# Performance work log

Measured on AMD Instinct MI355X. Metric: run time of the kernel, lower is better.

The kernel has to match this reference:

```python
import jax, jax.numpy as jnp
import numpy as np

B, N = 32, 2048
SLOTS, PSD, VIEW = 5, 15, 9
DM, NH, MH, EGO = 64, 4, 128, 32
PAIR_D = SLOTS * (SLOTS - 1) // 2          # 10
TER_D = VIEW * VIEW                        # 81
NBR_D = SLOTS * PSD + PAIR_D               # 85
D_OBS = EGO + NBR_D + TER_D                # 198


def setup_inputs() -> dict:
    key = jax.random.key(0)
    ks = jax.random.split(key, 64)

    def _p(k, shape, s=0.05):
        return (jax.random.normal(k, shape) * s).astype(jnp.float32)

    def z(*shape):
        return jnp.zeros(shape, jnp.float32)

    # --- observation with some genuinely-masked slots (r == 0) ---
    ego = jax.random.normal(ks[0], (B, N, EGO), jnp.float32)
    nbr = jax.random.normal(ks[1], (B, N, SLOTS, PSD), jnp.float32)
    keep = jax.random.bernoulli(ks[2], 0.8, (B, N, SLOTS)).astype(jnp.float32)
    nbr = jnp.concatenate([nbr[..., 0:3] * keep[..., None], nbr[..., 3:]], axis=-1)
    pair = jax.random.normal(ks[3], (B, N, PAIR_D), jnp.float32)
    ter = jax.random.normal(ks[4], (B, N, TER_D), jnp.float32)
    obs = jnp.concatenate([ego, nbr.reshape(B, N, SLOTS * PSD), pair, ter], axis=-1)

    i = 5
    def nk():
        nonlocal i
        i += 1
        return ks[i - 1]

    params = {
        "tok_w": _p(nk(), (12, DM)), "tok_b": z(DM),
        "ln1_s": jnp.ones((DM,), jnp.float32), "ln1_b": z(DM),
        "a1_qw": _p(nk(), (DM, DM)), "a1_qb": z(DM),
        "a1_kw": _p(nk(), (DM, DM)), "a1_kb": z(DM),
        "a1_vw": _p(nk(), (DM, DM)), "a1_vb": z(DM),
        "a1_ow": _p(nk(), (DM, DM)), "a1_ob": z(DM),
        "ln2_s": jnp.ones((DM,), jnp.float32), "ln2_b": z(DM),
        "m1_w": _p(nk(), (DM, MH)), "m1_b": z(MH),
        "m2_w": _p(nk(), (MH, MH)), "m2_b": z(MH),
        "m3_w": _p(nk(), (MH, DM)), "m3_b": z(DM),
        "e1_w": _p(nk(), (EGO, MH)), "e1_b": z(MH),
        "e2_w": _p(nk(), (MH, MH)), "e2_b": z(MH),
        "e3_w": _p(nk(), (MH, DM)), "e3_b": z(DM),
        "l1_w": _p(nk(), (2 * DM, MH)), "l1_b": z(MH),
        "l2_w": _p(nk(), (MH, MH)), "l2_b": z(MH),
        "l3_w": _p(nk(), (MH, 1)), "l3_b": z(1),
        "seed": _p(nk(), (1, 1, DM), 0.02),
        "p_qw": _p(nk(), (DM, DM)), "p_qb": z(DM),
        "p_kw": _p(nk(), (DM, DM)), "p_kb": z(DM),
        "p_vw": _p(nk(), (DM, DM)), "p_vb": z(DM),
        "p_ow": _p(nk(), (DM, DM)), "p_ob": z(DM),
        "pr_w": _p(nk(), (PAIR_D, DM)), "pr_b": z(DM),
        "h1_w": _p(nk(), (EGO + 2 * DM, MH)), "h1_b": z(MH),
        "h2_w": _p(nk(), (MH, MH)), "h2_b": z(MH),
        "h3_w": _p(nk(), (MH, MH)), "h3_b": z(MH),
    }
    return {"obs": obs, **params}


def _layernorm(x, s, b, eps=1e-6):
    m = jnp.mean(x, axis=-1, keepdims=True)
    v = jnp.var(x, axis=-1, keepdims=True)
    return (x - m) * jax.lax.rsqrt(v + eps) * s + b


def _zero_if_masked(x, mask):
    return jnp.where(mask[..., None], x, jnp.array(0.0, x.dtype))


def _masked_softmax(logits, mask, eps=1e-9):
    mask = mask.astype(bool)
    very_neg = jnp.array(-1e9, logits.dtype)
    ml = jnp.where(mask, logits, very_neg)
    mx = jnp.max(ml, axis=-1, keepdims=True)
    ex = jnp.exp(ml - mx) * mask.astype(logits.dtype)
    return ex / (jnp.sum(ex, axis=-1, keepdims=True) + eps)


def _mha(q_in, kv_in, attn_mask, qw, qb, kw, kb, vw, vb, ow, ob, nh=NH):
    dm = q_in.shape[-1]
    dh = dm // nh
    q = (q_in @ qw + qb).reshape(*q_in.shape[:-1], nh, dh)
    k = (kv_in @ kw + kb).reshape(*kv_in.shape[:-1], nh, dh)
    v = (kv_in @ vw + vb).reshape(*kv_in.shape[:-1], nh, dh)
    logits = jnp.einsum('...qhd,...khd->...hqk', q, k) / jnp.sqrt(jnp.float32(dh))
    neg = jnp.finfo(logits.dtype).min
    logits = jnp.where(attn_mask, logits, neg)
    attn = jax.nn.softmax(logits, axis=-1)
    o = jnp.einsum('...hqk,...khd->...qhd', attn, v).reshape(*q_in.shape[:-1], dm)
    return o @ ow + ob


def _mlp3(x, w1, b1, w2, b2, w3, b3):
    x = jax.nn.gelu(x @ w1 + b1)
    x = jax.nn.gelu(x @ w2 + b2)
    return x @ w3 + b3


def reference(obs, tok_w, tok_b, ln1_s, ln1_b,
              a1_qw, a1_qb, a1_kw, a1_kb, a1_vw, a1_vb, a1_ow, a1_ob,
              ln2_s, ln2_b, m1_w, m1_b, m2_w, m2_b, m3_w, m3_b,
              e1_w, e1_b, e2_w, e2_b, e3_w, e3_b,
              l1_w, l1_b, l2_w, l2_b, l3_w, l3_b,
              seed, p_qw, p_qb, p_kw, p_kb, p_vw, p_vb, p_ow, p_ob,
              pr_w, pr_b, h1_w, h1_b, h2_w, h2_b, h3_w, h3_b):
    obs = obs.astype(jnp.float32)
    Bb, Nn, Dd = obs.shape
    ego = obs[..., :EGO]
    nbr_all = obs[..., EGO:EGO + NBR_D]
    nbr_main = nbr_all[..., :SLOTS * PSD].reshape(Bb, Nn, SLOTS, PSD)
    pair = nbr_all[..., SLOTS * PSD:]

    r = nbr_main[..., 0:3]
    u = nbr_main[..., 3:6]
    att = nbr_main[..., 6:9]
    fre = nbr_main[..., 9:10]
    tem = nbr_main[..., 10:11]
    inv = nbr_main[..., 11:15]

    mask = jnp.any(jnp.abs(r) > 1e-6, axis=-1)                 # (B,N,K)
    mask_any = jnp.any(mask, axis=-1, keepdims=True)           # (B,N,1)
    mask_safe = jnp.where(mask_any, mask, mask.at[..., 0].set(True))

    r_clean = jnp.nan_to_num(r, nan=0.0, posinf=0.0, neginf=0.0)
    diff = r_clean[..., :, None, :] - r_clean[..., None, :, :]
    dist = jnp.linalg.norm(diff, axis=-1)                      # (B,N,K,K)
    pair_mask = mask[..., :, None] & mask[..., None, :]
    eye = jnp.eye(SLOTS, dtype=bool)[None, None]
    valid = pair_mask & ~eye
    big = jnp.array(1e9, dist.dtype)
    dist_no_self = jnp.where(eye, big, dist)
    d_min = jnp.min(jnp.where(valid, dist_no_self, big), axis=-1, keepdims=True)
    d_sum = jnp.sum(jnp.where(valid, dist, 0.0), axis=-1, keepdims=True)
    cnt = jnp.sum(valid, axis=-1, keepdims=True).astype(dist.dtype)
    d_mean = jnp.where(cnt > 0, d_sum / (cnt + 1e-9), 0.0)
    att_norm = jnp.linalg.norm(att, axis=-1, keepdims=True)

    tok_in = jnp.concatenate([inv, fre, tem, att, att_norm, d_min, d_mean], axis=-1)  # (B,N,K,12)
    tok = jax.nn.gelu(tok_in @ tok_w + tok_b)
    tok = _zero_if_masked(tok, mask)

    # --- SetTransformerBlock ---
    qk = mask_safe[..., :, None] & mask_safe[..., None, :]
    attn_mask = qk[..., None, :, :]                            # (B,N,1,K,K)
    y = _layernorm(tok, ln1_s, ln1_b)
    y = _mha(y, y, attn_mask, a1_qw, a1_qb, a1_kw, a1_kb, a1_vw, a1_vb, a1_ow, a1_ob)
    y = _zero_if_masked(y, mask)
    tok = tok + y
    zz = _layernorm(tok, ln2_s, ln2_b)
    zz = _mlp3(zz, m1_w, m1_b, m2_w, m2_b, m3_w, m3_b)
    zz = _zero_if_masked(zz, mask)
    tok = _zero_if_masked(tok + zz, mask)

    # --- alpha weights ---
    ego_ctx = _mlp3(ego, e1_w, e1_b, e2_w, e2_b, e3_w, e3_b)   # (B,N,DM)
    ego_ctx_b = jnp.broadcast_to(ego_ctx[..., None, :], tok.shape)
    logits = _mlp3(jnp.concatenate([tok, ego_ctx_b], axis=-1),
                   l1_w, l1_b, l2_w, l2_b, l3_w, l3_b)[..., 0]
    alpha = _masked_softmax(logits, mask)
    alpha3 = alpha[..., None]
    v_r = jnp.sum(alpha3 * r, axis=-2)
    v_u = jnp.sum(alpha3 * u, axis=-2)

    # --- AttentionPool ---
    q = jnp.broadcast_to(seed, (*tok.shape[:-2], 1, DM)).astype(jnp.float32)
    pool_mask = mask_safe[..., None, None, :]                  # (B,N,1,1,K)
    c = _mha(q, tok, pool_mask, p_qw, p_qb, p_kw, p_kb, p_vw, p_vb, p_ow, p_ob)[..., 0, :]
    c = jnp.where(mask_any, c, jnp.zeros_like(c))

    pair_emb = jax.nn.gelu(pair @ pr_w + pr_b)
    h_in = jnp.concatenate([ego, c, pair_emb], axis=-1)
    h = _mlp3(h_in, h1_w, h1_b, h2_w, h2_b, h3_w, h3_b)
    return jnp.concatenate([h, v_r, v_u], axis=-1)             # (B,N,134)
```

## Files before the change

kernel.cpp:

```cpp
#include <hip/hip_runtime.h>
#include <math.h>


#define DOBS 198
#define NEG_INF_F (-3.402823466e38f)

typedef __bf16 v8bf __attribute__((ext_vector_type(8)));
typedef __bf16 v4bf __attribute__((ext_vector_type(4)));
typedef float  v4f  __attribute__((ext_vector_type(4)));

struct P {
  const float *obs,*tok_w,*tok_b,*ln1_s,*ln1_b,
    *a1_qw,*a1_qb,*a1_kw,*a1_kb,*a1_vw,*a1_vb,*a1_ow,*a1_ob,
    *ln2_s,*ln2_b,*m1_w,*m1_b,*m2_w,*m2_b,*m3_w,*m3_b,
    *e1_w,*e1_b,*e2_w,*e2_b,*e3_w,*e3_b,
    *l1_w,*l1_b,*l2_w,*l2_b,*l3_w,*l3_b,
    *seed,*p_qw,*p_qb,*p_kw,*p_kb,*p_vw,*p_vb,*p_ow,*p_ob,
    *pr_w,*pr_b,*h1_w,*h1_b,*h2_w,*h2_b,*h3_w,*h3_b;
  float* out;
};
static_assert(sizeof(P) == 51*sizeof(void*), "P layout");

#define W_A1Q 0
#define W_A1K 4096
#define W_A1V 8192
#define W_A1O 12288
#define W_M1  16384
#define W_M2  24576
#define W_M3  40960
#define W_E1  49152
#define W_E2  53248
#define W_E3  69632
#define W_L1  77824
#define W_L2  94208
#define W_PK  110592
#define W_PV  114688
#define W_PO  118784
#define W_H1  122880
#define W_H2  143360
#define W_H3  159744
#define W_END 176128
#define W_QP  176128

__global__ __launch_bounds__(256)
void prep_w(P a, __bf16* ws)
{
  if (blockIdx.x == 172){
    int t = threadIdx.x;
    if (t < 64){
      float acc = a.p_qb[t];
      for (int k=0;k<64;k++) acc += a.seed[k]*a.p_qw[k*64+t];
      ((float*)(ws + W_QP))[t] = acc;
    }
    return;
  }
  const float* srcs[18] = {a.a1_qw,a.a1_kw,a.a1_vw,a.a1_ow,a.m1_w,a.m2_w,a.m3_w,
                           a.e1_w,a.e2_w,a.e3_w,a.l1_w,a.l2_w,a.p_kw,a.p_vw,a.p_ow,
                           a.h1_w,a.h2_w,a.h3_w};
  const int Ks[18]   = {64,64,64,64,64,128,128,32,128,128,128,128,64,64,64,160,128,128};
  const int Ns[18]   = {64,64,64,64,128,128,64,128,128,64,128,128,64,64,64,128,128,128};
  const int offs[18] = {W_A1Q,W_A1K,W_A1V,W_A1O,W_M1,W_M2,W_M3,W_E1,W_E2,W_E3,
                        W_L1,W_L2,W_PK,W_PV,W_PO,W_H1,W_H2,W_H3};
  __shared__ float tile[32][33];
  int b = blockIdx.x, m = 0, acc = 0;
  for (; m < 18; m++){
    int t = (Ks[m]/32)*(Ns[m]/32);
    if (b < acc + t) break;
    acc += t;
  }
  int lt = b - acc, K = Ks[m], N = Ns[m];
  int ntile = N/32, kt = lt/ntile, nt = lt%ntile;
  int tx = threadIdx.x & 31, ty = threadIdx.x >> 5;
  const float* S = srcs[m];
  #pragma unroll
  for (int rr=0; rr<32; rr+=8)
    tile[ty+rr][tx] = S[(size_t)(kt*32+ty+rr)*N + nt*32+tx];
  __syncthreads();
  __bf16* D = ws + offs[m];
  #pragma unroll
  for (int rr=0; rr<32; rr+=8)
    D[(size_t)(nt*32+ty+rr)*K + kt*32+tx] = (__bf16)tile[tx][ty+rr];
}

__device__ __forceinline__ float gelu_f(float x){
  float t = x * fmaf(0.0356774081f, x*x, 0.7978845608f);
  float u = __builtin_amdgcn_exp2f(-2.885390082f * t);
  return x * __builtin_amdgcn_rcpf(1.0f + u);
}

__device__ __forceinline__ void load16f(const __bf16* p, float* f){
  v8bf a = *(const v8bf*)p, b = *(const v8bf*)(p+8);
  #pragma unroll
  for (int i=0;i<8;i++){ f[i]=(float)a[i]; f[8+i]=(float)b[i]; }
}

template<int KT,int MT,int NTPW,typename LA,typename E>
__device__ __forceinline__ void gemmNS(LA la, const __bf16* __restrict__ Wt,
    const float* __restrict__ bias, int wv, int lane, E epi)
{
  const int ar = lane&15, quad = lane>>4;
  #pragma unroll
  for (int ln=0; ln<NTPW; ln++){
    const int wt = wv*NTPW + ln;
    const __bf16* wp = Wt + (size_t)(wt*16+ar)*(KT*32) + quad*8;
    v8bf wf[KT];
    #pragma unroll
    for (int kt=0;kt<KT;kt++) wf[kt] = *(const v8bf*)(wp + kt*32);
    float4 b4 = *(const float4*)(bias + wt*16 + quad*4);
    #pragma unroll
    for (int mt=0; mt<MT; mt++){
      v4f c; c[0]=b4.x; c[1]=b4.y; c[2]=b4.z; c[3]=b4.w;
      #pragma unroll
      for (int kt=0;kt<KT;kt++)
        c = __builtin_amdgcn_mfma_f32_16x16x32_bf16(wf[kt], la(mt,kt,ar,quad), c, 0,0,0);
      epi(wt*16 + quad*4, mt, ar, c);
    }
  }
}

__global__ __launch_bounds__(256,3)
void swarm_mfma(P a, const __bf16* __restrict__ ws, int ntok)
{
  __shared__ char smem[53120] __attribute__((aligned(16)));
  __bf16* Ab   = (__bf16*)(smem);
  __bf16* Bb   = (__bf16*)(smem+17408);
  float*  TOKIN= (float*) (smem+17408);
  __bf16* Tk   = (__bf16*)(smem+34816);
  float*  OBSf = (float*) (smem+34816);
  __bf16* Po   = (__bf16*)(smem+34816);
  __bf16* Pe   = (__bf16*)(smem+44032);
  __bf16* Eg   = (__bf16*)(smem+46080);
  __bf16* Ru   = (__bf16*)(smem+47360);
  __bf16* mfb  = (__bf16*)(smem+48096);
  __bf16* msfb = (__bf16*)(smem+48224);
  float*  many = (float*) (smem+48352);
  float*  lga  = (float*) (smem+48416);
  __bf16* ECX  = (__bf16*)(smem+48672);
  float*  pattn= (float*) (smem+48672);
  __bf16* ATTb = (__bf16*)(smem+50720);
  __bf16* Cc   = (__bf16*)(smem+50720);

  const int lane = threadIdx.x & 63;
  const int wv   = threadIdx.x >> 6;
  const int ar   = lane & 15, quad = lane >> 4;
  const long blkT0 = (long)blockIdx.x*12;

  for (int it=lane; it<3*117; it+=64){
    int tg=it/117, c=it-tg*117;
    long gt = blkT0 + 3*wv + tg; if (gt>ntok-1) gt=ntok-1;
    OBSf[(3*wv+tg)*120+c] = a.obs[gt*DOBS+c];
  }
  float* Df = (float*)Ab;
  for (int it=lane; it<75; it+=64){
    int tg=it/25, p=it-tg*25, i=p/5, j=p-i*5;
    const float* ob = OBSf + (3*wv+tg)*120 + 32;
    float d2=0.f;
    #pragma unroll
    for (int d=0;d<3;d++){
      float ri=ob[15*i+d]; ri = isfinite(ri)?ri:0.f;
      float rj=ob[15*j+d]; rj = isfinite(rj)?rj:0.f;
      float df=ri-rj; d2 += df*df;
    }
    Df[(3*wv+tg)*32+p]=sqrtf(d2);
  }
  if (lane<15){
    int T=3*wv+lane/5, s=lane%5;
    const float* b = OBSf + T*120 + 32 + 15*s;
    mfb[15*wv+lane] = (__bf16)((fabsf(b[0])>1e-6f||fabsf(b[1])>1e-6f||fabsf(b[2])>1e-6f)?1.f:0.f);
  }
  if (wv==0 && lane>=60){ mfb[lane]=(__bf16)0.f; msfb[lane]=(__bf16)0.f; }
  if (wv==0 && lane>=12 && lane<16) many[lane]=0.f;
  if (lane<3){
    int T=3*wv+lane;
    float any = (float)mfb[T*5]+(float)mfb[T*5+1]+(float)mfb[T*5+2]+(float)mfb[T*5+3]+(float)mfb[T*5+4];
    float anyf = (any>0.f)?1.f:0.f; many[T]=anyf;
    #pragma unroll
    for (int i=0;i<5;i++) msfb[T*5+i] = (anyf>0.f)? mfb[T*5+i] : (__bf16)((i==0)?1.f:0.f);
  }
  if (lane<15){
    int T=3*wv+lane/5, i=lane%5, R=15*wv+lane;
    float dmin=1e9f,dsum=0.f,cnt=0.f;
    #pragma unroll
    for (int j=0;j<5;j++){
      if (j!=i && (float)mfb[T*5+i]>0.5f && (float)mfb[T*5+j]>0.5f){
        float dd=Df[T*32+i*5+j];
        dmin=fminf(dmin,dd); dsum+=dd; cnt+=1.f;
      }
    }
    TOKIN[R*12+10]=dmin;
    TOKIN[R*12+11]=(cnt>0.f)? dsum/(cnt+1e-9f) : 0.f;
  }
  for (int it=lane; it<150; it+=64){
    int tg=it/50, q=it-tg*50, s=q/10, c=q-s*10;
    int T=3*wv+tg;
    const float* b = OBSf + T*120 + 32 + 15*s;
    float v;
    if (c<4)        v=b[11+c];
    else if (c==4)  v=b[9];
    else if (c==5)  v=b[10];
    else if (c<9)   v=b[6+(c-6)];
    else { float a0=b[6],a1=b[7],a2=b[8]; v=sqrtf(a0*a0+a1*a1+a2*a2); }
    TOKIN[(T*5+s)*12+c]=v;
  }
  for (int it=lane; it<96; it+=64){
    int tg=it>>5, c=it&31;
    Eg[(3*wv+tg)*40+c] = (__bf16)OBSf[(3*wv+tg)*120+c];
  }
  for (int it=lane; it<90; it+=64){
    int tg=it/30, c=it-tg*30;
    Ru[(3*wv+tg)*30+c] = (__bf16)OBSf[(3*wv+tg)*120+32+15*(c/6)+(c%6)];
  }
  for (int it=lane; it<192; it+=64){
    int tg=it>>6, c=it&63;
    float acc = a.pr_b[c];
    #pragma unroll
    for (int k=0;k<10;k++) acc += OBSf[(3*wv+tg)*120+107+k]*a.pr_w[k*64+c];
    Pe[(3*wv+tg)*64+c] = (__bf16)gelu_f(acc);
  }
  __syncthreads();

  {
    float w0[12];
    #pragma unroll
    for (int k=0;k<12;k++) w0[k] = a.tok_w[k*64+lane];
    float tb = a.tok_b[lane];
    for (int r=0;r<15;r++){
      int R = 15*wv + r;
      const float4* tin = (const float4*)(TOKIN + R*12);
      float4 x0 = tin[0], x1 = tin[1], x2 = tin[2];
      float acc = tb;
      acc=fmaf(x0.x,w0[0],acc); acc=fmaf(x0.y,w0[1],acc);
      acc=fmaf(x0.z,w0[2],acc); acc=fmaf(x0.w,w0[3],acc);
      acc=fmaf(x1.x,w0[4],acc); acc=fmaf(x1.y,w0[5],acc);
      acc=fmaf(x1.z,w0[6],acc); acc=fmaf(x1.w,w0[7],acc);
      acc=fmaf(x2.x,w0[8],acc); acc=fmaf(x2.y,w0[9],acc);
      acc=fmaf(x2.z,w0[10],acc); acc=fmaf(x2.w,w0[11],acc);
      Tk[R*72+lane] = (__bf16)(gelu_f(acc)*(float)mfb[R]);
    }
  }
  if (ar<15){
    int R = 15*wv + ar;
    float x[16]; load16f(Tk + R*72 + quad*16, x);
    float s=0.f;
    #pragma unroll
    for (int i=0;i<16;i++) s += x[i];
    s += __shfl_xor(s,16,64); s += __shfl_xor(s,32,64);
    float m = s*(1.f/64.f), q=0.f;
    #pragma unroll
    for (int i=0;i<16;i++){ float d=x[i]-m; q=fmaf(d,d,q); }
    q += __shfl_xor(q,16,64); q += __shfl_xor(q,32,64);
    float rs = __builtin_amdgcn_rsqf(q*(1.f/64.f)+1e-6f);
    v8bf o0,o1;
    #pragma unroll
    for (int i=0;i<8;i++){
      o0[i]=(__bf16)((x[i]  -m)*rs*a.ln1_s[quad*16+i]  +a.ln1_b[quad*16+i]);
      o1[i]=(__bf16)((x[8+i]-m)*rs*a.ln1_s[quad*16+8+i]+a.ln1_b[quad*16+8+i]);
    }
    *(v8bf*)(Ab+R*136+quad*16)=o0; *(v8bf*)(Ab+R*136+quad*16+8)=o1;
  }
  __syncthreads();

  auto actAb = [&](int mt,int kt,int r,int q){ return *(const v8bf*)(Ab + (size_t)(mt*16+r)*136 + q*8 + kt*32); };
  auto actBb = [&](int mt,int kt,int r,int q){ return *(const v8bf*)(Bb + (size_t)(mt*16+r)*136 + q*8 + kt*32); };
  auto actTk = [&](int mt,int kt,int r,int q){ return *(const v8bf*)(Tk + (size_t)(mt*16+r)*72  + q*8 + kt*32); };

  gemmNS<2,4,1>(actAb, ws+W_A1K, a.a1_kb, wv, lane,
    [&](int wb,int mt,int r,v4f c){ v4bf o;
      #pragma unroll
      for (int k=0;k<4;k++) o[k]=(__bf16)c[k];
      *(v4bf*)&Bb[(mt*16+r)*136+64+wb]=o; });
  gemmNS<2,4,1>(actAb, ws+W_A1V, a.a1_vb, wv, lane,
    [&](int wb,int mt,int r,v4f c){ v4bf o;
      #pragma unroll
      for (int k=0;k<4;k++) o[k]=(__bf16)c[k];
      *(v4bf*)&Ab[(mt*16+r)*136+64+wb]=o; });
  gemmNS<2,4,1>(actAb, ws+W_A1Q, a.a1_qb, wv, lane,
    [&](int wb,int mt,int r,v4f c){ v4bf o;
      #pragma unroll
      for (int k=0;k<4;k++) o[k]=(__bf16)c[k];
      *(v4bf*)&Bb[(mt*16+r)*136+wb]=o; });
  __syncthreads();

  if (lane<60){
    int tg=lane/20, rem=lane-tg*20, h=rem/5, i=rem-h*5;
    int T=3*wv+tg;
    bool mi = (float)msfb[T*5+i]>0.5f;
    float qv[16]; load16f(&Bb[(T*5+i)*136 + h*16], qv);
    float lgv[5], mx=NEG_INF_F;
    #pragma unroll
    for (int j=0;j<5;j++){
      float kk[16]; load16f(&Bb[(T*5+j)*136 + 64 + h*16], kk);
      float d=0.f;
      #pragma unroll
      for (int dd=0;dd<16;dd++) d += qv[dd]*kk[dd];
      bool mj = (float)msfb[T*5+j]>0.5f;
      lgv[j] = (mi&&mj)? d*0.25f : NEG_INF_F;
      mx = fmaxf(mx,lgv[j]);
    }
    float sum=0.f, ex[5];
    #pragma unroll
    for (int j=0;j<5;j++){ ex[j]=__expf(lgv[j]-mx); sum+=ex[j]; }
    float inv=1.0f/sum;
    #pragma unroll
    for (int j=0;j<5;j++) ATTb[T*100+(h*5+i)*5+j]=(__bf16)(ex[j]*inv);
  }
  {
    int h = lane>>4;
    #pragma unroll
    for (int tg=0; tg<3; tg++){
      int T=3*wv+tg;
      float v5[5];
      #pragma unroll
      for (int j=0;j<5;j++) v5[j] = (float)Ab[(T*5+j)*136+64+lane];
      #pragma unroll
      for (int i=0;i<5;i++){
        float o=0.f;
        #pragma unroll
        for (int j=0;j<5;j++) o += (float)ATTb[T*100+(h*5+i)*5+j]*v5[j];
        Ab[(T*5+i)*136+lane]=(__bf16)o;
      }
    }
  }
  __syncthreads();

  gemmNS<2,4,1>(actAb, ws+W_A1O, a.a1_ob, wv, lane,
    [&](int wb,int mt,int r,v4f c){
      int R=mt*16+r; float mm=(float)mfb[R];
      v4bf old=*(const v4bf*)&Tk[R*72+wb]; v4bf o;
      #pragma unroll
      for (int k=0;k<4;k++) o[k]=(__bf16)((float)old[k]+c[k]*mm);
      *(v4bf*)&Tk[R*72+wb]=o; });
  __syncthreads();

  if (ar<15){
    int R = 15*wv + ar;
    float x[16]; load16f(Tk + R*72 + quad*16, x);
    float s=0.f;
    #pragma unroll
    for (int i=0;i<16;i++) s += x[i];
    s += __shfl_xor(s,16,64); s += __shfl_xor(s,32,64);
    float m = s*(1.f/64.f), q=0.f;
    #pragma unroll
    for (int i=0;i<16;i++){ float d=x[i]-m; q=fmaf(d,d,q); }
    q += __shfl_xor(q,16,64); q += __shfl_xor(q,32,64);
    float rs = __builtin_amdgcn_rsqf(q*(1.f/64.f)+1e-6f);
    v8bf o0,o1;
    #pragma unroll
    for (int i=0;i<8;i++){
      o0[i]=(__bf16)((x[i]  -m)*rs*a.ln2_s[quad*16+i]  +a.ln2_b[quad*16+i]);
      o1[i]=(__bf16)((x[8+i]-m)*rs*a.ln2_s[quad*16+8+i]+a.ln2_b[quad*16+8+i]);
    }
    *(v8bf*)(Ab+R*136+quad*16)=o0; *(v8bf*)(Ab+R*136+quad*16+8)=o1;
  }
  __syncthreads();

  gemmNS<2,4,2>(actAb, ws+W_M1, a.m1_b, wv, lane,
    [&](int wb,int mt,int r,v4f c){ v4bf o;
      #pragma unroll
      for (int k=0;k<4;k++) o[k]=(__bf16)gelu_f(c[k]);
      *(v4bf*)&Bb[(mt*16+r)*136+wb]=o; });
  __syncthreads();
  gemmNS<4,4,2>(actBb, ws+W_M2, a.m2_b, wv, lane,
    [&](int wb,int mt,int r,v4f c){ v4bf o;
      #pragma unroll
      for (int k=0;k<4;k++) o[k]=(__bf16)gelu_f(c[k]);
      *(v4bf*)&Ab[(mt*16+r)*136+wb]=o; });
  __syncthreads();
  gemmNS<4,4,1>(actAb, ws+W_M3, a.m3_b, wv, lane,
    [&](int wb,int mt,int r,v4f c){
      int R=mt*16+r; float mm=(float)mfb[R];
      v4bf old=*(const v4bf*)&Tk[R*72+wb]; v4bf o;
      #pragma unroll
      for (int k=0;k<4;k++) o[k]=(__bf16)(((float)old[k]+c[k]*mm)*mm);
      *(v4bf*)&Tk[R*72+wb]=o; });
  gemmNS<1,1,2>([&](int,int,int r,int q){ return *(const v8bf*)(Eg + (size_t)r*40 + q*8); },
    ws+W_E1, a.e1_b, wv, lane,
    [&](int wb,int mt,int r,v4f c){ v4bf o;
      #pragma unroll
      for (int k=0;k<4;k++) o[k]=(__bf16)gelu_f(c[k]);
      *(v4bf*)&Bb[r*136+wb]=o; });
  __syncthreads();
  gemmNS<4,1,2>(actBb, ws+W_E2, a.e2_b, wv, lane,
    [&](int wb,int mt,int r,v4f c){ v4bf o;
      #pragma unroll
      for (int k=0;k<4;k++) o[k]=(__bf16)gelu_f(c[k]);
      *(v4bf*)&Ab[r*136+wb]=o; });
  __syncthreads();
  gemmNS<4,1,1>(actAb, ws+W_E3, a.e3_b, wv, lane,
    [&](int wb,int mt,int r,v4f c){ v4bf o;
      #pragma unroll
      for (int k=0;k<4;k++) o[k]=(__bf16)c[k];
      *(v4bf*)&ECX[r*64+wb]=o; });
  __syncthreads();
  gemmNS<4,4,2>([&](int mt,int kt,int r,int q){
      int R=mt*16+r;
      return (kt<2) ? *(const v8bf*)(Tk + (size_t)R*72 + q*8 + kt*32)
                    : *(const v8bf*)(ECX + (size_t)((R*205)>>10)*64 + q*8 + (kt-2)*32); },
    ws+W_L1, a.l1_b, wv, lane,
    [&](int wb,int mt,int r,v4f c){ v4bf o;
      #pragma unroll
      for (int k=0;k<4;k++) o[k]=(__bf16)gelu_f(c[k]);
      *(v4bf*)&Bb[(mt*16+r)*136+wb]=o; });
  __syncthreads();
  gemmNS<4,4,2>(actBb, ws+W_L2, a.l2_b, wv, lane,
    [&](int wb,int mt,int r,v4f c){ v4bf o;
      #pragma unroll
      for (int k=0;k<4;k++) o[k]=(__bf16)gelu_f(c[k]);
      *(v4bf*)&Ab[(mt*16+r)*136+wb]=o; });
  __syncthreads();

  if (ar<15){
    int R = 15*wv + ar;
    float x[16], y[16];
    load16f(&Ab[R*136 + quad*32], x);
    load16f(&Ab[R*136 + quad*32 + 16], y);
    const float* w = a.l3_w + quad*32;
    float p = 0.f;
    #pragma unroll
    for (int i=0;i<16;i++) p = fmaf(x[i], w[i], p);
    #pragma unroll
    for (int i=0;i<16;i++) p = fmaf(y[i], w[16+i], p);
    p += __shfl_xor(p,16,64); p += __shfl_xor(p,32,64);
    if (quad==0) lga[R] = p + a.l3_b[0];
  }
  gemmNS<2,4,1>(actTk, ws+W_PK, a.p_kb, wv, lane,
    [&](int wb,int mt,int r,v4f c){ v4bf o;
      #pragma unroll
      for (int k=0;k<4;k++) o[k]=(__bf16)c[k];
      *(v4bf*)&Bb[(mt*16+r)*136+wb]=o; });
  gemmNS<2,4,1>(actTk, ws+W_PV, a.p_vb, wv, lane,
    [&](int wb,int mt,int r,v4f c){ v4bf o;
      #pragma unroll
      for (int k=0;k<4;k++) o[k]=(__bf16)c[k];
      *(v4bf*)&Bb[(mt*16+r)*136+64+wb]=o; });
  if (lane<3){
    int T=3*wv+lane;
    float ml[5], mx=-1e9f;
    #pragma unroll
    for (int i=0;i<5;i++){ ml[i]=((float)mfb[T*5+i]>0.5f)? lga[T*5+i] : -1e9f; mx=fmaxf(mx,ml[i]); }
    float den=0.f, e[5];
    #pragma unroll
    for (int i=0;i<5;i++){ e[i]=__expf(ml[i]-mx)*(float)mfb[T*5+i]; den+=e[i]; }
    float inv=1.0f/(den+1e-9f);
    #pragma unroll
    for (int i=0;i<5;i++) lga[T*5+i]=e[i]*inv;
  }
  if (lane<18){
    int tg=lane/6, c=lane-tg*6;
    int T=3*wv+tg;
    float v=0.f;
    #pragma unroll
    for (int i=0;i<5;i++) v += lga[T*5+i]*(float)Ru[T*30+i*6+c];
    long tk = blkT0 + T;
    if (tk<ntok) a.out[tk*134+128+c]=v;
  }
  __syncthreads();

  if (lane<12){
    const float* qg = (const float*)(ws + W_QP);
    int tg=lane>>2, h=lane&3;
    int T=3*wv+tg;
    float qv[16];
    #pragma unroll
    for (int dd=0;dd<16;dd++) qv[dd]=qg[h*16+dd];
    float lgv[5], mx=NEG_INF_F;
    #pragma unroll
    for (int j=0;j<5;j++){
      float kk[16]; load16f(&Bb[(T*5+j)*136 + h*16], kk);
      float d=0.f;
      #pragma unroll
      for (int dd=0;dd<16;dd++) d += qv[dd]*kk[dd];
      lgv[j] = ((float)msfb[T*5+j]>0.5f)? d*0.25f : NEG_INF_F;
      mx = fmaxf(mx,lgv[j]);
    }
    float sum=0.f, ex[5];
    #pragma unroll
    for (int j=0;j<5;j++){ ex[j]=__expf(lgv[j]-mx); sum+=ex[j]; }
    float inv=1.0f/sum;
    #pragma unroll
    for (int j=0;j<5;j++) pattn[T*20+h*5+j]=ex[j]*inv;
  }
  for (int it=lane; it<192; it+=64){
    int tg=it>>6, c=it&63, h=c>>4;
    int T=3*wv+tg;
    float o=0.f;
    #pragma unroll
    for (int j=0;j<5;j++)
      o += pattn[T*20+h*5+j]*(float)Bb[(T*5+j)*136+64+c];
    Po[T*64+c]=(__bf16)o;
  }
  __syncthreads();

  gemmNS<2,1,1>([&](int,int kt,int r,int q){ return *(const v8bf*)(Po + (size_t)r*64 + q*8 + kt*32); },
    ws+W_PO, a.p_ob, wv, lane,
    [&](int wb,int mt,int r,v4f c){
      float mm = many[r];
      v4bf o;
      #pragma unroll
      for (int k=0;k<4;k++) o[k]=(__bf16)(c[k]*mm);
      *(v4bf*)&Cc[r*64+wb]=o; });
  __syncthreads();

  gemmNS<5,1,2>([&](int,int kt,int r,int q){
      if (kt==0) return *(const v8bf*)(Eg + (size_t)r*40 + q*8);
      if (kt<3)  return *(const v8bf*)(Cc + (size_t)r*64 + q*8 + (kt-1)*32);
      return *(const v8bf*)(Pe + (size_t)r*64 + q*8 + (kt-3)*32); },
    ws+W_H1, a.h1_b, wv, lane,
    [&](int wb,int mt,int r,v4f c){ v4bf o;
      #pragma unroll
      for (int k=0;k<4;k++) o[k]=(__bf16)gelu_f(c[k]);
      *(v4bf*)&Bb[r*136+wb]=o; });
  __syncthreads();
  gemmNS<4,1,2>(actBb, ws+W_H2, a.h2_b, wv, lane,
    [&](int wb,int mt,int r,v4f c){ v4bf o;
      #pragma unroll
      for (int k=0;k<4;k++) o[k]=(__bf16)gelu_f(c[k]);
      *(v4bf*)&Ab[r*136+wb]=o; });
  __syncthreads();
  gemmNS<4,1,2>(actAb, ws+W_H3, a.h3_b, wv, lane,
    [&](int wb,int mt,int r,v4f c){
      long tk = blkT0 + r;
      if (r<12 && tk<ntok){
        float2* o2 = (float2*)&a.out[tk*134 + wb];
        o2[0] = make_float2(c[0], c[1]);
        o2[1] = make_float2(c[2], c[3]);
      } });
}

extern "C" void kernel_launch(void* const* d_in, const int* in_sizes, int n_in,
                              void* d_out, int out_size, void* d_ws, size_t ws_size,
                              hipStream_t stream)
{
  P a;
  const float** pp = reinterpret_cast<const float**>(&a);
  for (int i=0;i<50;i++) pp[i] = reinterpret_cast<const float*>(d_in[i]);
  a.out = reinterpret_cast<float*>(d_out);
  int ntok = in_sizes[0] / DOBS;

  __bf16* ws = reinterpret_cast<__bf16*>(d_ws);
  hipLaunchKernelGGL(prep_w, dim3(173), dim3(256), 0, stream, a, ws);
  hipLaunchKernelGGL(swarm_mfma, dim3((ntok+11)/12), dim3(256), 0, stream, a, ws, ntok);
}
```

Measured before the change: 513.3 us.

## Split GEMM work across M and N per wave and fuse QKV/KV projections

The shared MFMA GEMM helper is generalized so each wave takes a 2D (M-group × N-group) tile and can process several weight matrices in one pass. Each activation fragment loaded from LDS is then reused across multiple N tiles and weights. The attention Q/K/V projections and the pooling K/V projections are fused into single calls, and the larger MLP GEMMs now give each wave more N tiles over half the M tiles. This cuts redundant LDS activation reads and adds MFMA independence per load, at the cost of more live registers per wave, which may hurt occupancy under launch_bounds(256,3).

Result: slower. 601.7 us (+17.2%).

```diff
diff --git a/kernel.cpp b/kernel.cpp
--- a/kernel.cpp
+++ b/kernel.cpp
@@ -94,28 +94,63 @@
   for (int i=0;i<8;i++){ f[i]=(float)a[i]; f[8+i]=(float)b[i]; }
 }
 
-template<int KT,int MT,int NTPW,typename LA,typename E>
-__device__ __forceinline__ void gemmNS(LA la, const __bf16* __restrict__ Wt,
-    const float* __restrict__ bias, int wv, int lane, E epi)
+template<int KT,int MT,int NTPW,int MSPL,int NW,typename LA,typename E>
+__device__ __forceinline__ void gemmNS(LA la, const __bf16* const* Ws,
+    const float* const* bs, int wv, int lane, E epi)
 {
+  static_assert(MT % MSPL == 0, "MT % MSPL");
   const int ar = lane&15, quad = lane>>4;
+  constexpr int NWN = 4/MSPL;
+  constexpr int SH  = (NWN==4)?2:((NWN==2)?1:0);
+  constexpr int MTW = MT/MSPL;
+  const int ng = wv & (NWN-1), mg = wv >> SH;
+  v8bf  wf[NW][NTPW][KT];
+  float4 b4[NW][NTPW];
+  #pragma unroll
+  for (int w=0; w<NW; w++)
   #pragma unroll
   for (int ln=0; ln<NTPW; ln++){
-    const int wt = wv*NTPW + ln;
-    const __bf16* wp = Wt + (size_t)(wt*16+ar)*(KT*32) + quad*8;
-    v8bf wf[KT];
-    #pragma unroll
-    for (int kt=0;kt<KT;kt++) wf[kt] = *(const v8bf*)(wp + kt*32);
-    float4 b4 = *(const float4*)(bias + wt*16 + quad*4);
-    #pragma unroll
-    for (int mt=0; mt<MT; mt++){
-      v4f c; c[0]=b4.x; c[1]=b4.y; c[2]=b4.z; c[3]=b4.w;
-      #pragma unroll
-      for (int kt=0;kt<KT;kt++)
-        c = __builtin_amdgcn_mfma_f32_16x16x32_bf16(wf[kt], la(mt,kt,ar,quad), c, 0,0,0);
-      epi(wt*16 + quad*4, mt, ar, c);
-    }
-  }
+    const int wt = ng*NTPW + ln;
+    const __bf16* wp = Ws[w] + (size_t)(wt*16+ar)*(KT*32) + quad*8;
+    #pragma unroll
+    for (int kt=0;kt<KT;kt++) wf[w][ln][kt] = *(const v8bf*)(wp + kt*32);
+    b4[w][ln] = *(const float4*)(bs[w] + wt*16 + quad*4);
+  }
+  #pragma unroll
+  for (int mi=0; mi<MTW; mi++){
+    const int mt = mg*MTW + mi;
+    v4f c[NW][NTPW];
+    #pragma unroll
+    for (int w=0;w<NW;w++)
+    #pragma unroll
+    for (int ln=0;ln<NTPW;ln++){
+      c[w][ln][0]=b4[w][ln].x; c[w][ln][1]=b4[w][ln].y;
+      c[w][ln][2]=b4[w][ln].z; c[w][ln][3]=b4[w][ln].w;
+    }
+    #pragma unroll
+    for (int kt=0;kt<KT;kt++){
+      v8bf av = la(mt,kt,ar,quad);
+      #pragma unroll
+      for (int w=0;w<NW;w++)
+      #pragma unroll
+      for (int ln=0;ln<NTPW;ln++)
+        c[w][ln] = __builtin_amdgcn_mfma_f32_16x16x32_bf16(wf[w][ln][kt], av, c[w][ln], 0,0,0);
+    }
+    #pragma unroll
+    for (int w=0;w<NW;w++)
+    #pragma unroll
+    for (int ln=0;ln<NTPW;ln++)
+      epi(w, (ng*NTPW+ln)*16 + quad*4, mt, ar, c[w][ln]);
+  }
+}
+
+template<int KT,int MT,int NTPW,int MSPL,typename LA,typename E>
+__device__ __forceinline__ void gemm1(LA la, const __bf16* W, const float* b,
+    int wv, int lane, E epi)
+{
+  const __bf16* Ws[1] = {W}; const float* bs[1] = {b};
+  gemmNS<KT,MT,NTPW,MSPL,1>(la, Ws, bs, wv, lane,
+    [&](int, int wb,int mt,int r,v4f c){ epi(wb,mt,r,c); });
 }
 
 __global__ __launch_bounds__(256,3)
@@ -264,21 +299,18 @@
   auto actBb = [&](int mt,int kt,int r,int q){ return *(const v8bf*)(Bb + (size_t)(mt*16+r)*136 + q*8 + kt*32); };
   auto actTk = [&](int mt,int kt,int r,int q){ return *(const v8bf*)(Tk + (size_t)(mt*16+r)*72  + q*8 + kt*32); };
 
-  gemmNS<2,4,1>(actAb, ws+W_A1K, a.a1_kb, wv, lane,
-    [&](int wb,int mt,int r,v4f c){ v4bf o;
-      #pragma unroll
-      for (int k=0;k<4;k++) o[k]=(__bf16)c[k];
-      *(v4bf*)&Bb[(mt*16+r)*136+64+wb]=o; });
-  gemmNS<2,4,1>(actAb, ws+W_A1V, a.a1_vb, wv, lane,
-    [&](int wb,int mt,int r,v4f c){ v4bf o;
-      #pragma unroll
-      for (int k=0;k<4;k++) o[k]=(__bf16)c[k];
-      *(v4bf*)&Ab[(mt*16+r)*136+64+wb]=o; });
-  gemmNS<2,4,1>(actAb, ws+W_A1Q, a.a1_qb, wv, lane,
-    [&](int wb,int mt,int r,v4f c){ v4bf o;
-      #pragma unroll
-      for (int k=0;k<4;k++) o[k]=(__bf16)c[k];
-      *(v4bf*)&Bb[(mt*16+r)*136+wb]=o; });
+  {
+    const __bf16* Ws[3] = {ws+W_A1K, ws+W_A1V, ws+W_A1Q};
+    const float*  bs[3] = {a.a1_kb, a.a1_vb, a.a1_qb};
+    gemmNS<2,4,2,2,3>(actAb, Ws, bs, wv, lane,
+      [&](int w,int wb,int mt,int r,v4f c){ v4bf o;
+        #pragma unroll
+        for (int k=0;k<4;k++) o[k]=(__bf16)c[k];
+        __bf16* d = (w==0)? &Bb[(mt*16+r)*136+64+wb]
+                 : (w==1)? &Ab[(mt*16+r)*136+64+wb]
+                         : &Bb[(mt*16+r)*136+wb];
+        *(v4bf*)d = o; });
+  }
   __syncthreads();
 
   if (lane<60){
@@ -323,7 +355,7 @@
   }
   __syncthreads();
 
-  gemmNS<2,4,1>(actAb, ws+W_A1O, a.a1_ob, wv, lane,
+  gemm1<2,4,2,2>(actAb, ws+W_A1O, a.a1_ob, wv, lane,
     [&](int wb,int mt,int r,v4f c){
       int R=mt*16+r; float mm=(float)mfb[R];
       v4bf old=*(const v4bf*)&Tk[R*72+wb]; v4bf o;
@@ -354,45 +386,45 @@
   }
   __syncthreads();
 
-  gemmNS<2,4,2>(actAb, ws+W_M1, a.m1_b, wv, lane,
+  gemm1<2,4,4,2>(actAb, ws+W_M1, a.m1_b, wv, lane,
     [&](int wb,int mt,int r,v4f c){ v4bf o;
       #pragma unroll
       for (int k=0;k<4;k++) o[k]=(__bf16)gelu_f(c[k]);
       *(v4bf*)&Bb[(mt*16+r)*136+wb]=o; });
   __syncthreads();
-  gemmNS<4,4,2>(actBb, ws+W_M2, a.m2_b, wv, lane,
+  gemm1<4,4,4,2>(actBb, ws+W_M2, a.m2_b, wv, lane,
     [&](int wb,int mt,int r,v4f c){ v4bf o;
       #pragma unroll
       for (int k=0;k<4;k++) o[k]=(__bf16)gelu_f(c[k]);
       *(v4bf*)&Ab[(mt*16+r)*136+wb]=o; });
   __syncthreads();
-  gemmNS<4,4,1>(actAb, ws+W_M3, a.m3_b, wv, lane,
+  gemm1<4,4,2,2>(actAb, ws+W_M3, a.m3_b, wv, lane,
     [&](int wb,int mt,int r,v4f c){
       int R=mt*16+r; float mm=(float)mfb[R];
       v4bf old=*(const v4bf*)&Tk[R*72+wb]; v4bf o;
       #pragma unroll
       for (int k=0;k<4;k++) o[k]=(__bf16)(((float)old[k]+c[k]*mm)*mm);
       *(v4bf*)&Tk[R*72+wb]=o; });
-  gemmNS<1,1,2>([&](int,int,int r,int q){ return *(const v8bf*)(Eg + (size_t)r*40 + q*8); },
+  gemm1<1,1,2,1>([&](int,int,int r,int q){ return *(const v8bf*)(Eg + (size_t)r*40 + q*8); },
     ws+W_E1, a.e1_b, wv, lane,
     [&](int wb,int mt,int r,v4f c){ v4bf o;
       #pragma unroll
       for (int k=0;k<4;k++) o[k]=(__bf16)gelu_f(c[k]);
       *(v4bf*)&Bb[r*136+wb]=o; });
   __syncthreads();
-  gemmNS<4,1,2>(actBb, ws+W_E2, a.e2_b, wv, lane,
+  gemm1<4,1,2,1>(actBb, ws+W_E2, a.e2_b, wv, lane,
     [&](int wb,int mt,int r,v4f c){ v4bf o;
       #pragma unroll
       for (int k=0;k<4;k++) o[k]=(__bf16)gelu_f(c[k]);
       *(v4bf*)&Ab[r*136+wb]=o; });
   __syncthreads();
-  gemmNS<4,1,1>(actAb, ws+W_E3, a.e3_b, wv, lane,
+  gemm1<4,1,1,1>(actAb, ws+W_E3, a.e3_b, wv, lane,
     [&](int wb,int mt,int r,v4f c){ v4bf o;
       #pragma unroll
       for (int k=0;k<4;k++) o[k]=(__bf16)c[k];
       *(v4bf*)&ECX[r*64+wb]=o; });
   __syncthreads();
-  gemmNS<4,4,2>([&](int mt,int kt,int r,int q){
+  gemm1<4,4,4,2>([&](int mt,int kt,int r,int q){
       int R=mt*16+r;
       return (kt<2) ? *(const v8bf*)(Tk + (size_t)R*72 + q*8 + kt*32)
                     : *(const v8bf*)(ECX + (size_t)((R*205)>>10)*64 + q*8 + (kt-2)*32); },
@@ -402,7 +434,7 @@
       for (int k=0;k<4;k++) o[k]=(__bf16)gelu_f(c[k]);
       *(v4bf*)&Bb[(mt*16+r)*136+wb]=o; });
   __syncthreads();
-  gemmNS<4,4,2>(actBb, ws+W_L2, a.l2_b, wv, lane,
+  gemm1<4,4,4,2>(actBb, ws+W_L2, a.l2_b, wv, lane,
     [&](int wb,int mt,int r,v4f c){ v4bf o;
       #pragma unroll
       for (int k=0;k<4;k++) o[k]=(__bf16)gelu_f(c[k]);
@@ -423,16 +455,15 @@
     p += __shfl_xor(p,16,64); p += __shfl_xor(p,32,64);
     if (quad==0) lga[R] = p + a.l3_b[0];
   }
-  gemmNS<2,4,1>(actTk, ws+W_PK, a.p_kb, wv, lane,
-    [&](int wb,int mt,int r,v4f c){ v4bf o;
-      #pragma unroll
-      for (int k=0;k<4;k++) o[k]=(__bf16)c[k];
-      *(v4bf*)&Bb[(mt*16+r)*136+wb]=o; });
-  gemmNS<2,4,1>(actTk, ws+W_PV, a.p_vb, wv, lane,
-    [&](int wb,int mt,int r,v4f c){ v4bf o;
-      #pragma unroll
-      for (int k=0;k<4;k++) o[k]=(__bf16)c[k];
-      *(v4bf*)&Bb[(mt*16+r)*136+64+wb]=o; });
+  {
+    const __bf16* Ws[2] = {ws+W_PK, ws+W_PV};
+    const float*  bs[2] = {a.p_kb, a.p_vb};
+    gemmNS<2,4,2,2,2>(actTk, Ws, bs, wv, lane,
+      [&](int w,int wb,int mt,int r,v4f c){ v4bf o;
+        #pragma unroll
+        for (int k=0;k<4;k++) o[k]=(__bf16)c[k];
+        *(v4bf*)&Bb[(mt*16+r)*136 + (w?64:0) + wb] = o; });
+  }
   if (lane<3){
     int T=3*wv+lane;
     float ml[5], mx=-1e9f;
@@ -491,7 +522,7 @@
   }
   __syncthreads();
 
-  gemmNS<2,1,1>([&](int,int kt,int r,int q){ return *(const v8bf*)(Po + (size_t)r*64 + q*8 + kt*32); },
+  gemm1<2,1,1,1>([&](int,int kt,int r,int q){ return *(const v8bf*)(Po + (size_t)r*64 + q*8 + kt*32); },
     ws+W_PO, a.p_ob, wv, lane,
     [&](int wb,int mt,int r,v4f c){
       float mm = many[r];
@@ -501,7 +532,7 @@
       *(v4bf*)&Cc[r*64+wb]=o; });
   __syncthreads();
 
-  gemmNS<5,1,2>([&](int,int kt,int r,int q){
+  gemm1<5,1,2,1>([&](int,int kt,int r,int q){
       if (kt==0) return *(const v8bf*)(Eg + (size_t)r*40 + q*8);
       if (kt<3)  return *(const v8bf*)(Cc + (size_t)r*64 + q*8 + (kt-1)*32);
       return *(const v8bf*)(Pe + (size_t)r*64 + q*8 + (kt-3)*32); },
@@ -511,13 +542,13 @@
       for (int k=0;k<4;k++) o[k]=(__bf16)gelu_f(c[k]);
       *(v4bf*)&Bb[r*136+wb]=o; });
   __syncthreads();
-  gemmNS<4,1,2>(actBb, ws+W_H2, a.h2_b, wv, lane,
+  gemm1<4,1,2,1>(actBb, ws+W_H2, a.h2_b, wv, lane,
     [&](int wb,int mt,int r,v4f c){ v4bf o;
       #pragma unroll
       for (int k=0;k<4;k++) o[k]=(__bf16)gelu_f(c[k]);
       *(v4bf*)&Ab[r*136+wb]=o; });
   __syncthreads();
-  gemmNS<4,1,2>(actAb, ws+W_H3, a.h3_b, wv, lane,
+  gemm1<4,1,2,1>(actAb, ws+W_H3, a.h3_b, wv, lane,
     [&](int wb,int mt,int r,v4f c){
       long tk = blkT0 + r;
       if (r<12 && tk<ntok){
```

## Prefetch next GEMM weights across barriers and use lgkm-only barrier

Applied to the files above, without the earlier changes.

Splits the GEMM helper into a weight/bias register load and a compute step, and issues each stage's weight load before the preceding barrier so global latency overlaps the sync and earlier work. Replaces __syncthreads with a barrier that waits only on LDS counters (lgkmcnt), so outstanding global weight loads need not drain at each barrier. This raises register pressure, since several weight fragments are held live at once, which may hurt occupancy under launch_bounds(256,3).

Measured after the change: 497.9 us. 3.0% less time.

```diff
diff --git a/kernel.cpp b/kernel.cpp
--- a/kernel.cpp
+++ b/kernel.cpp
@@ -4,6 +4,9 @@
 
 #define DOBS 198
 #define NEG_INF_F (-3.402823466e38f)
+
+#define BAR() do { asm volatile("s_waitcnt lgkmcnt(0)" ::: "memory"); \
+                   __builtin_amdgcn_s_barrier(); } while(0)
 
 typedef __bf16 v8bf __attribute__((ext_vector_type(8)));
 typedef __bf16 v4bf __attribute__((ext_vector_type(4)));
@@ -94,25 +97,42 @@
   for (int i=0;i<8;i++){ f[i]=(float)a[i]; f[8+i]=(float)b[i]; }
 }
 
+template<int KT,int NTPW> struct WF {
+  v8bf  w[NTPW][KT];
+  float4 b[NTPW];
+};
+
+template<int KT,int NTPW>
+__device__ __forceinline__ WF<KT,NTPW> wload(const __bf16* __restrict__ Wt,
+    const float* __restrict__ bias, int wv, int lane)
+{
+  WF<KT,NTPW> f;
+  const int ar = lane&15, quad = lane>>4;
+  #pragma unroll
+  for (int ln=0; ln<NTPW; ln++){
+    const int wt = wv*NTPW + ln;
+    const __bf16* wp = Wt + (size_t)(wt*16+ar)*(KT*32) + quad*8;
+    #pragma unroll
+    for (int kt=0;kt<KT;kt++) f.w[ln][kt] = *(const v8bf*)(wp + kt*32);
+    f.b[ln] = *(const float4*)(bias + wt*16 + quad*4);
+  }
+  return f;
+}
+
 template<int KT,int MT,int NTPW,typename LA,typename E>
-__device__ __forceinline__ void gemmNS(LA la, const __bf16* __restrict__ Wt,
-    const float* __restrict__ bias, int wv, int lane, E epi)
+__device__ __forceinline__ void gemmW(LA la, const WF<KT,NTPW>& f,
+    int wv, int lane, E epi)
 {
   const int ar = lane&15, quad = lane>>4;
   #pragma unroll
   for (int ln=0; ln<NTPW; ln++){
     const int wt = wv*NTPW + ln;
-    const __bf16* wp = Wt + (size_t)(wt*16+ar)*(KT*32) + quad*8;
-    v8bf wf[KT];
-    #pragma unroll
-    for (int kt=0;kt<KT;kt++) wf[kt] = *(const v8bf*)(wp + kt*32);
-    float4 b4 = *(const float4*)(bias + wt*16 + quad*4);
     #pragma unroll
     for (int mt=0; mt<MT; mt++){
-      v4f c; c[0]=b4.x; c[1]=b4.y; c[2]=b4.z; c[3]=b4.w;
+      v4f c; c[0]=f.b[ln].x; c[1]=f.b[ln].y; c[2]=f.b[ln].z; c[3]=f.b[ln].w;
       #pragma unroll
       for (int kt=0;kt<KT;kt++)
-        c = __builtin_amdgcn_mfma_f32_16x16x32_bf16(wf[kt], la(mt,kt,ar,quad), c, 0,0,0);
+        c = __builtin_amdgcn_mfma_f32_16x16x32_bf16(f.w[ln][kt], la(mt,kt,ar,quad), c, 0,0,0);
       epi(wt*16 + quad*4, mt, ar, c);
     }
   }
@@ -217,7 +237,9 @@
     for (int k=0;k<10;k++) acc += OBSf[(3*wv+tg)*120+107+k]*a.pr_w[k*64+c];
     Pe[(3*wv+tg)*64+c] = (__bf16)gelu_f(acc);
   }
-  __syncthreads();
+  BAR();
+
+  auto wfK = wload<2,1>(ws+W_A1K, a.a1_kb, wv, lane);
 
   {
     float w0[12];
@@ -258,28 +280,31 @@
     }
     *(v8bf*)(Ab+R*136+quad*16)=o0; *(v8bf*)(Ab+R*136+quad*16+8)=o1;
   }
-  __syncthreads();
+  BAR();
 
   auto actAb = [&](int mt,int kt,int r,int q){ return *(const v8bf*)(Ab + (size_t)(mt*16+r)*136 + q*8 + kt*32); };
   auto actBb = [&](int mt,int kt,int r,int q){ return *(const v8bf*)(Bb + (size_t)(mt*16+r)*136 + q*8 + kt*32); };
   auto actTk = [&](int mt,int kt,int r,int q){ return *(const v8bf*)(Tk + (size_t)(mt*16+r)*72  + q*8 + kt*32); };
 
-  gemmNS<2,4,1>(actAb, ws+W_A1K, a.a1_kb, wv, lane,
+  auto wfV = wload<2,1>(ws+W_A1V, a.a1_vb, wv, lane);
+  auto wfQ = wload<2,1>(ws+W_A1Q, a.a1_qb, wv, lane);
+  gemmW<2,4,1>(actAb, wfK, wv, lane,
     [&](int wb,int mt,int r,v4f c){ v4bf o;
       #pragma unroll
       for (int k=0;k<4;k++) o[k]=(__bf16)c[k];
       *(v4bf*)&Bb[(mt*16+r)*136+64+wb]=o; });
-  gemmNS<2,4,1>(actAb, ws+W_A1V, a.a1_vb, wv, lane,
+  gemmW<2,4,1>(actAb, wfV, wv, lane,
     [&](int wb,int mt,int r,v4f c){ v4bf o;
       #pragma unroll
       for (int k=0;k<4;k++) o[k]=(__bf16)c[k];
       *(v4bf*)&Ab[(mt*16+r)*136+64+wb]=o; });
-  gemmNS<2,4,1>(actAb, ws+W_A1Q, a.a1_qb, wv, lane,
+  gemmW<2,4,1>(actAb, wfQ, wv, lane,
     [&](int wb,int mt,int r,v4f c){ v4bf o;
       #pragma unroll
       for (int k=0;k<4;k++) o[k]=(__bf16)c[k];
       *(v4bf*)&Bb[(mt*16+r)*136+wb]=o; });
-  __syncthreads();
+  auto wfO = wload<2,1>(ws+W_A1O, a.a1_ob, wv, lane);
+  BAR();
 
   if (lane<60){
     int tg=lane/20, rem=lane-tg*20, h=rem/5, i=rem-h*5;
@@ -321,16 +346,17 @@
       }
     }
   }
-  __syncthreads();
-
-  gemmNS<2,4,1>(actAb, ws+W_A1O, a.a1_ob, wv, lane,
+  BAR();
+
+  gemmW<2,4,1>(actAb, wfO, wv, lane,
     [&](int wb,int mt,int r,v4f c){
       int R=mt*16+r; float mm=(float)mfb[R];
       v4bf old=*(const v4bf*)&Tk[R*72+wb]; v4bf o;
       #pragma unroll
       for (int k=0;k<4;k++) o[k]=(__bf16)((float)old[k]+c[k]*mm);
       *(v4bf*)&Tk[R*72+wb]=o; });
-  __syncthreads();
+  auto wfM1 = wload<2,2>(ws+W_M1, a.m1_b, wv, lane);
+  BAR();
 
   if (ar<15){
     int R = 15*wv + ar;
@@ -352,62 +378,71 @@
     }
     *(v8bf*)(Ab+R*136+quad*16)=o0; *(v8bf*)(Ab+R*136+quad*16+8)=o1;
   }
-  __syncthreads();
-
-  gemmNS<2,4,2>(actAb, ws+W_M1, a.m1_b, wv, lane,
+  BAR();
+
+  gemmW<2,4,2>(actAb, wfM1, wv, lane,
     [&](int wb,int mt,int r,v4f c){ v4bf o;
       #pragma unroll
       for (int k=0;k<4;k++) o[k]=(__bf16)gelu_f(c[k]);
       *(v4bf*)&Bb[(mt*16+r)*136+wb]=o; });
-  __syncthreads();
-  gemmNS<4,4,2>(actBb, ws+W_M2, a.m2_b, wv, lane,
+  auto wfM2 = wload<4,2>(ws+W_M2, a.m2_b, wv, lane);
+  BAR();
+  gemmW<4,4,2>(actBb, wfM2, wv, lane,
     [&](int wb,int mt,int r,v4f c){ v4bf o;
       #pragma unroll
       for (int k=0;k<4;k++) o[k]=(__bf16)gelu_f(c[k]);
       *(v4bf*)&Ab[(mt*16+r)*136+wb]=o; });
-  __syncthreads();
-  gemmNS<4,4,1>(actAb, ws+W_M3, a.m3_b, wv, lane,
+  auto wfM3 = wload<4,1>(ws+W_M3, a.m3_b, wv, lane);
+  auto wfE1 = wload<1,2>(ws+W_E1, a.e1_b, wv, lane);
+  BAR();
+  gemmW<4,4,1>(actAb, wfM3, wv, lane,
     [&](int wb,int mt,int r,v4f c){
       int R=mt*16+r; float mm=(float)mfb[R];
       v4bf old=*(const v4bf*)&Tk[R*72+wb]; v4bf o;
       #pragma unroll
       for (int k=0;k<4;k++) o[k]=(__bf16)(((float)old[k]+c[k]*mm)*mm);
       *(v4bf*)&Tk[R*72+wb]=o; });
-  gemmNS<1,1,2>([&](int,int,int r,int q){ return *(const v8bf*)(Eg + (size_t)r*40 + q*8); },
-    ws+W_E1, a.e1_b, wv, lane,
+  gemmW<1,1,2>([&](int,int,int r,int q){ return *(const v8bf*)(Eg + (size_t)r*40 + q*8); },
+    wfE1, wv, lane,
     [&](int wb,int mt,int r,v4f c){ v4bf o;
       #pragma unroll
       for (int k=0;k<4;k++) o[k]=(__bf16)gelu_f(c[k]);
       *(v4bf*)&Bb[r*136+wb]=o; });
-  __syncthreads();
-  gemmNS<4,1,2>(actBb, ws+W_E2, a.e2_b, wv, lane,
+  auto wfE2 = wload<4,2>(ws+W_E2, a.e2_b, wv, lane);
+  BAR();
+  gemmW<4,1,2>(actBb, wfE2, wv, lane,
     [&](int wb,int mt,int r,v4f c){ v4bf o;
       #pragma unroll
       for (int k=0;k<4;k++) o[k]=(__bf16)gelu_f(c[k]);
       *(v4bf*)&Ab[r*136+wb]=o; });
-  __syncthreads();
-  gemmNS<4,1,1>(actAb, ws+W_E3, a.e3_b, wv, lane,
+  auto wfE3 = wload<4,1>(ws+W_E3, a.e3_b, wv, lane);
+  BAR();
+  gemmW<4,1,1>(actAb, wfE3, wv, lane,
     [&](int wb,int mt,int r,v4f c){ v4bf o;
       #pragma unroll
       for (int k=0;k<4;k++) o[k]=(__bf16)c[k];
       *(v4bf*)&ECX[r*64+wb]=o; });
-  __syncthreads();
-  gemmNS<4,4,2>([&](int mt,int kt,int r,int q){
+  auto wfL1 = wload<4,2>(ws+W_L1, a.l1_b, wv, lane);
+  BAR();
+  gemmW<4,4,2>([&](int mt,int kt,int r,int q){
       int R=mt*16+r;
       return (kt<2) ? *(const v8bf*)(Tk + (size_t)R*72 + q*8 + kt*32)
                     : *(const v8bf*)(ECX + (size_t)((R*205)>>10)*64 + q*8 + (kt-2)*32); },
-    ws+W_L1, a.l1_b, wv, lane,
+    wfL1, wv, lane,
     [&](int wb,int mt,int r,v4f c){ v4bf o;
       #pragma unroll
       for (int k=0;k<4;k++) o[k]=(__bf16)gelu_f(c[k]);
       *(v4bf*)&Bb[(mt*16+r)*136+wb]=o; });
-  __syncthreads();
-  gemmNS<4,4,2>(actBb, ws+W_L2, a.l2_b, wv, lane,
+  auto wfL2 = wload<4,2>(ws+W_L2, a.l2_b, wv, lane);
+  BAR();
+  gemmW<4,4,2>(actBb, wfL2, wv, lane,
     [&](int wb,int mt,int r,v4f c){ v4bf o;
       #pragma unroll
       for (int k=0;k<4;k++) o[k]=(__bf16)gelu_f(c[k]);
       *(v4bf*)&Ab[(mt*16+r)*136+wb]=o; });
-  __syncthreads();
+  auto wfPK = wload<2,1>(ws+W_PK, a.p_kb, wv, lane);
+  auto wfPV = wload<2,1>(ws+W_PV, a.p_vb, wv, lane);
+  BAR();
 
   if (ar<15){
     int R = 15*wv + ar;
@@ -423,12 +458,12 @@
     p += __shfl_xor(p,16,64); p += __shfl_xor(p,32,64);
     if (quad==0) lga[R] = p + a.l3_b[0];
   }
-  gemmNS<2,4,1>(actTk, ws+W_PK, a.p_kb, wv, lane,
+  gemmW<2,4,1>(actTk, wfPK, wv, lane,
     [&](int wb,int mt,int r,v4f c){ v4bf o;
       #pragma unroll
       for (int k=0;k<4;k++) o[k]=(__bf16)c[k];
       *(v4bf*)&Bb[(mt*16+r)*136+wb]=o; });
-  gemmNS<2,4,1>(actTk, ws+W_PV, a.p_vb, wv, lane,
+  gemmW<2,4,1>(actTk, wfPV, wv, lane,
     [&](int wb,int mt,int r,v4f c){ v4bf o;
       #pragma unroll
       for (int k=0;k<4;k++) o[k]=(__bf16)c[k];
@@ -454,7 +489,7 @@
     long tk = blkT0 + T;
     if (tk<ntok) a.out[tk*134+128+c]=v;
   }
-  __syncthreads();
+  BAR();
 
   if (lane<12){
     const float* qg = (const float*)(ws + W_QP);
@@ -489,35 +524,39 @@
       o += pattn[T*20+h*5+j]*(float)Bb[(T*5+j)*136+64+c];
     Po[T*64+c]=(__bf16)o;
   }
-  __syncthreads();
-
-  gemmNS<2,1,1>([&](int,int kt,int r,int q){ return *(const v8bf*)(Po + (size_t)r*64 + q*8 + kt*32); },
-    ws+W_PO, a.p_ob, wv, lane,
+  auto wfPO = wload<2,1>(ws+W_PO, a.p_ob, wv, lane);
+  BAR();
+
+  gemmW<2,1,1>([&](int,int kt,int r,int q){ return *(const v8bf*)(Po + (size_t)r*64 + q*8 + kt*32); },
+    wfPO, wv, lane,
     [&](int wb,int mt,int r,v4f c){
       float mm = many[r];
       v4bf o;
       #pragma unroll
       for (int k=0;k<4;k++) o[k]=(__bf16)(c[k]*mm);
       *(v4bf*)&Cc[r*64+wb]=o; });
-  __syncthreads();
-
-  gemmNS<5,1,2>([&](int,int kt,int r,int q){
+  auto wfH1 = wload<5,2>(ws+W_H1, a.h1_b, wv, lane);
+  BAR();
+
+  gemmW<5,1,2>([&](int,int kt,int r,int q){
       if (kt==0) return *(const v8bf*)(Eg + (size_t)r*40 + q*8);
       if (kt<3)  return *(const v8bf*)(Cc + (size_t)r*64 + q*8 + (kt-1)*32);
       return *(const v8bf*)(Pe + (size_t)r*64 + q*8 + (kt-3)*32); },
-    ws+W_H1, a.h1_b, wv, lane,
+    wfH1, wv, lane,
     [&](int wb,int mt,int r,v4f c){ v4bf o;
       #pragma unroll
       for (int k=0;k<4;k++) o[k]=(__bf16)gelu_f(c[k]);
       *(v4bf*)&Bb[r*136+wb]=o; });
-  __syncthreads();
-  gemmNS<4,1,2>(actBb, ws+W_H2, a.h2_b, wv, lane,
+  auto wfH2 = wload<4,2>(ws+W_H2, a.h2_b, wv, lane);
+  BAR();
+  gemmW<4,1,2>(actBb, wfH2, wv, lane,
     [&](int wb,int mt,int r,v4f c){ v4bf o;
       #pragma unroll
       for (int k=0;k<4;k++) o[k]=(__bf16)gelu_f(c[k]);
       *(v4bf*)&Ab[r*136+wb]=o; });
-  __syncthreads();
-  gemmNS<4,1,2>(actAb, ws+W_H3, a.h3_b, wv, lane,
+  auto wfH3 = wload<4,2>(ws+W_H3, a.h3_b, wv, lane);
+  BAR();
+  gemmW<4,1,2>(actAb, wfH3, wv, lane,
     [&](int wb,int mt,int r,v4f c){
       long tk = blkT0 + r;
       if (r<12 && tk<ntok){
```
